# Optimization experiments

Measured on AMD Instinct MI355X. Metric: run time of the kernel, lower is better.

The kernel has to match this reference:

```python
import jax, jax.numpy as jnp
import numpy as np

D_MODEL = 1024
N_HEADS = 16
D_K = D_MODEL // N_HEADS
ROPE_THETA = 10000.0


def setup_inputs() -> dict:
    key = jax.random.key(0)
    ks = jax.random.split(key, 5)
    B, S = 2, 2048
    scale = 1.0 / np.sqrt(D_MODEL)
    return {
        "x": jax.random.normal(ks[0], (B, S, D_MODEL), dtype=jnp.float32),
        "token_positions": jnp.arange(S, dtype=jnp.int32),
        "Wq": jax.random.normal(ks[1], (D_MODEL, D_MODEL), dtype=jnp.float32) * scale,
        "Wk": jax.random.normal(ks[2], (D_MODEL, D_MODEL), dtype=jnp.float32) * scale,
        "Wv": jax.random.normal(ks[3], (D_MODEL, D_MODEL), dtype=jnp.float32) * scale,
        "Wo": jax.random.normal(ks[4], (D_MODEL, D_MODEL), dtype=jnp.float32) * scale,
    }


def apply_rope(x, positions):
    # x: [b, h, s, d_k]; interleaved-pair rotary embedding, theta=10000
    half = D_K // 2
    inv_freq = ROPE_THETA ** (-jnp.arange(0, half, dtype=x.dtype) * 2.0 / D_K)  # [half]
    angles = positions.astype(x.dtype)[:, None] * inv_freq[None, :]             # [s, half]
    cos, sin = jnp.cos(angles), jnp.sin(angles)                                 # [s, half]
    x1 = x[..., 0::2]
    x2 = x[..., 1::2]
    r1 = x1 * cos - x2 * sin
    r2 = x1 * sin + x2 * cos
    # re-interleave
    return jnp.stack([r1, r2], axis=-1).reshape(x.shape)


def reference(x, token_positions, Wq, Wk, Wv, Wo):
    B, S, _ = x.shape
    # Linear(d_model, d_model) with no bias: y = x @ W.T
    Q = jnp.einsum("bsd,ed->bse", x, Wq).reshape(B, S, N_HEADS, D_K).transpose(0, 2, 1, 3)
    K = jnp.einsum("bsd,ed->bse", x, Wk).reshape(B, S, N_HEADS, D_K).transpose(0, 2, 1, 3)
    V = jnp.einsum("bsd,ed->bse", x, Wv).reshape(B, S, N_HEADS, D_K).transpose(0, 2, 1, 3)
    Q = apply_rope(Q, token_positions)
    K = apply_rope(K, token_positions)
    scores = jnp.einsum("bhqd,bhkd->bhqk", Q, K) / jnp.sqrt(jnp.asarray(D_K, x.dtype))
    causal = jnp.tril(jnp.ones((S, S), dtype=bool))
    scores = jnp.where(causal[None, None, :, :], scores, jnp.asarray(-jnp.inf, x.dtype))
    attn = jax.nn.softmax(scores, axis=-1)
    out = jnp.einsum("bhqk,bhkd->bhqd", attn, V)            # [b, h, s, d_k]
    out = out.transpose(0, 2, 1, 3).reshape(B, S, D_MODEL)   # [b, s, d_model]
    return jnp.einsum("bsd,ed->bse", out, Wo)
```

## Files before the change

### kernel.cpp

```cpp
#include <hip/hip_runtime.h>
#include <hip/hip_bf16.h>
#include <math.h>

#define SEQ 2048
#define NH  16
#define DKH 64
#define DM  1024
#define MR  4096

using bf16x8 = __attribute__((ext_vector_type(8))) short;
using f32x4  = __attribute__((ext_vector_type(4))) float;

__device__ __forceinline__ ushort f2b(float f) {
  unsigned u = __float_as_uint(f);
  return (ushort)((u + 0x7fffu + ((u >> 16) & 1u)) >> 16);
}

__device__ __forceinline__ float exp2_fast(float x) {
  float r; asm("v_exp_f32 %0, %1" : "=v"(r) : "v"(x)); return r;
}

__device__ __forceinline__ unsigned cvt_pk(float lo, float hi) {
  __hip_bfloat162 h = __float22bfloat162_rn(float2{lo, hi});
  return *reinterpret_cast<unsigned*>(&h);
}

__device__ __forceinline__ void gll16(const void* g, void* l) {
  __builtin_amdgcn_global_load_lds(
      (const __attribute__((address_space(1))) void*)g,
      (__attribute__((address_space(3))) void*)l, 16, 0, 0);
}

__global__ __launch_bounds__(256) void cvt_all(
    const float* __restrict__ x,  const float* __restrict__ wq,
    const float* __restrict__ wk, const float* __restrict__ wv,
    const float* __restrict__ wo,
    ushort* __restrict__ xb,  ushort* __restrict__ wqb, ushort* __restrict__ wkb,
    ushort* __restrict__ wvb, ushort* __restrict__ wob)
{
  size_t e = ((size_t)blockIdx.x * 256 + threadIdx.x) * 4;
  const float* s; ushort* d; size_t off;
  if      (e < 4194304) { s = x;  d = xb;  off = e; }
  else if (e < 5242880) { s = wq; d = wqb; off = e - 4194304; }
  else if (e < 6291456) { s = wk; d = wkb; off = e - 5242880; }
  else if (e < 7340032) { s = wv; d = wvb; off = e - 6291456; }
  else                  { s = wo; d = wob; off = e - 7340032; }
  float4 f = *(const float4*)(s + off);
  ushort4 o4 = { f2b(f.x), f2b(f.y), f2b(f.z), f2b(f.w) };
  *(ushort4*)(d + off) = o4;
}

__global__ __launch_bounds__(512) void gemm_qkv(
    const ushort* __restrict__ X,
    const ushort* __restrict__ Wq, const ushort* __restrict__ Wk, const ushort* __restrict__ Wv,
    ushort* __restrict__ Q, ushort* __restrict__ K, ushort* __restrict__ Vt,
    const int* __restrict__ pos)
{
  __shared__ __align__(16) char As[2][16384];
  __shared__ __align__(16) char Bs[2][16384];

  const int id  = blockIdx.x;
  const int xcd = id & 7;
  const int i   = id >> 3;
  const int mt  = xcd * 4 + (i & 3);
  const int nt  = i >> 2;
  const int m0  = mt * 128;
  const int nG  = nt * 128;
  const int z   = nG >> 10;
  const int n0  = nG & 1023;
  const ushort* W = (z == 0) ? Wq : (z == 1) ? Wk : Wv;

  const int tid  = threadIdx.x;
  const int lane = tid & 63;
  const int w    = tid >> 6;
  const int wm   = (w >> 2) * 64;
  const int wn   = (w & 3) * 32;
  const int li   = lane & 15;
  const int g    = lane >> 4;

  f32x4 acc[4][2] = {};

  auto stage = [&](int t, int buf) {
    const int k0 = t * 64;
    #pragma unroll
    for (int it = 0; it < 2; ++it) {
      const int L  = w * 2048 + it * 1024 + lane * 16;
      const int r  = L >> 7;
      const int sc = ((L >> 4) & 7) ^ (r & 7);
      gll16(X + (size_t)(m0 + r) * DM + k0 + sc * 8, &As[buf][w * 2048 + it * 1024]);
      gll16(W + (size_t)(n0 + r) * DM + k0 + sc * 8, &Bs[buf][w * 2048 + it * 1024]);
    }
  };

  auto compute = [&](int buf) {
    #pragma unroll
    for (int ks = 0; ks < 2; ++ks) {
      bf16x8 af[4], bfr[2];
      #pragma unroll
      for (int mf = 0; mf < 4; ++mf) {
        const int row = wm + mf * 16 + li;
        af[mf] = *(const bf16x8*)(&As[buf][row * 128 + (((ks * 4 + g) ^ (row & 7)) << 4)]);
      }
      #pragma unroll
      for (int nf = 0; nf < 2; ++nf) {
        const int row = wn + nf * 16 + li;
        bfr[nf] = *(const bf16x8*)(&Bs[buf][row * 128 + (((ks * 4 + g) ^ (row & 7)) << 4)]);
      }
      #pragma unroll
      for (int mf = 0; mf < 4; ++mf)
        #pragma unroll
        for (int nf = 0; nf < 2; ++nf)
          acc[mf][nf] = __builtin_amdgcn_mfma_f32_16x16x32_bf16(af[mf], bfr[nf], acc[mf][nf], 0, 0, 0);
    }
  };

  stage(0, 0);
  for (int t = 0; t < 16; ++t) {
    if (t < 15) {
      stage(t + 1, (t + 1) & 1);
      __builtin_amdgcn_sched_barrier(0);
      asm volatile("s_waitcnt vmcnt(4)" ::: "memory");
    } else {
      asm volatile("s_waitcnt vmcnt(0)" ::: "memory");
    }
    __builtin_amdgcn_s_barrier();
    __builtin_amdgcn_sched_barrier(0);
    compute(t & 1);
    __builtin_amdgcn_sched_barrier(0);
    __builtin_amdgcn_s_barrier();
  }

  #pragma unroll
  for (int nf = 0; nf < 2; ++nf) {
    const int n = n0 + wn + nf * 16 + li;
    const int h = n >> 6;
    const int d = n & 63;
    if (z == 2) {
      #pragma unroll
      for (int mf = 0; mf < 4; ++mf) {
        const int m  = m0 + wm + mf * 16 + g * 4;
        const int b  = m >> 11;
        const int s2 = m & (SEQ - 1);
        ushort4 pk = { f2b(acc[mf][nf][0]), f2b(acc[mf][nf][1]),
                       f2b(acc[mf][nf][2]), f2b(acc[mf][nf][3]) };
        *(ushort4*)(Vt + (((size_t)b * NH + h) * DKH + d) * SEQ + s2) = pk;
      }
    } else {
      ushort* DST = (z == 0) ? Q : K;
      const float freq = __expf(-(float)(d >> 1) * 0.2878231366242557f);
      #pragma unroll
      for (int mf = 0; mf < 4; ++mf) {
        #pragma unroll
        for (int r = 0; r < 4; ++r) {
          const int m  = m0 + wm + mf * 16 + g * 4 + r;
          const int b  = m >> 11;
          const int s2 = m & (SEQ - 1);
          const float ang = (float)pos[s2] * freq;
          float sn, cs;
          __sincosf(ang, &sn, &cs);
          const float v1 = acc[mf][nf][r];
          const float v2 = __shfl_xor(v1, 1);
          float ov = (d & 1) ? (v2 * sn + v1 * cs)
                             : (v1 * cs - v2 * sn);
          if (z == 0) ov *= 0.1803368801111204f;
          DST[(((size_t)b * NH + h) * SEQ + s2) * DKH + d] = f2b(ov);
        }
      }
    }
  }
}

__global__ __launch_bounds__(512) void gemm_wo(
    const ushort* __restrict__ A, const ushort* __restrict__ W,
    float* __restrict__ out)
{
  __shared__ __align__(16) char As[2][16384];
  __shared__ __align__(16) char Bs[2][16384];

  const int id  = blockIdx.x;
  const int xcd = id & 7;
  const int i   = id >> 3;
  const int mt  = xcd * 4 + (i & 3);
  const int nt  = i >> 2;
  const int m0  = mt * 128;
  const int n0  = nt * 128;

  const int tid  = threadIdx.x;
  const int lane = tid & 63;
  const int w    = tid >> 6;
  const int wm   = (w >> 2) * 64;
  const int wn   = (w & 3) * 32;
  const int li   = lane & 15;
  const int g    = lane >> 4;

  f32x4 acc[4][2] = {};

  auto stage = [&](int t, int buf) {
    const int k0 = t * 64;
    #pragma unroll
    for (int it = 0; it < 2; ++it) {
      const int L  = w * 2048 + it * 1024 + lane * 16;
      const int r  = L >> 7;
      const int sc = ((L >> 4) & 7) ^ (r & 7);
      gll16(A + (size_t)(m0 + r) * DM + k0 + sc * 8, &As[buf][w * 2048 + it * 1024]);
      gll16(W + (size_t)(n0 + r) * DM + k0 + sc * 8, &Bs[buf][w * 2048 + it * 1024]);
    }
  };

  auto compute = [&](int buf) {
    #pragma unroll
    for (int ks = 0; ks < 2; ++ks) {
      bf16x8 af[4], bfr[2];
      #pragma unroll
      for (int mf = 0; mf < 4; ++mf) {
        const int row = wm + mf * 16 + li;
        af[mf] = *(const bf16x8*)(&As[buf][row * 128 + (((ks * 4 + g) ^ (row & 7)) << 4)]);
      }
      #pragma unroll
      for (int nf = 0; nf < 2; ++nf) {
        const int row = wn + nf * 16 + li;
        bfr[nf] = *(const bf16x8*)(&Bs[buf][row * 128 + (((ks * 4 + g) ^ (row & 7)) << 4)]);
      }
      #pragma unroll
      for (int mf = 0; mf < 4; ++mf)
        #pragma unroll
        for (int nf = 0; nf < 2; ++nf)
          acc[mf][nf] = __builtin_amdgcn_mfma_f32_16x16x32_bf16(af[mf], bfr[nf], acc[mf][nf], 0, 0, 0);
    }
  };

  stage(0, 0);
  for (int t = 0; t < 16; ++t) {
    if (t < 15) {
      stage(t + 1, (t + 1) & 1);
      __builtin_amdgcn_sched_barrier(0);
      asm volatile("s_waitcnt vmcnt(4)" ::: "memory");
    } else {
      asm volatile("s_waitcnt vmcnt(0)" ::: "memory");
    }
    __builtin_amdgcn_s_barrier();
    __builtin_amdgcn_sched_barrier(0);
    compute(t & 1);
    __builtin_amdgcn_sched_barrier(0);
    __builtin_amdgcn_s_barrier();
  }

  #pragma unroll
  for (int nf = 0; nf < 2; ++nf)
    #pragma unroll
    for (int mf = 0; mf < 4; ++mf)
      #pragma unroll
      for (int r = 0; r < 4; ++r)
        out[(size_t)(m0 + wm + mf * 16 + g * 4 + r) * DM + n0 + wn + nf * 16 + li] = acc[mf][nf][r];
}

__global__ __launch_bounds__(256) void attn(
    const ushort* __restrict__ Q, const ushort* __restrict__ K,
    const ushort* __restrict__ Vt, ushort* __restrict__ AO)
{
  __shared__ __align__(16) char Ks[8192];
  __shared__ __align__(16) char Vs[8192];
  __shared__ __align__(16) char Ps[8192];

  const int tid  = threadIdx.x;
  const int lane = tid & 63;
  const int w    = tid >> 6;
  const int li   = lane & 15;
  const int g    = lane >> 4;

  const int bx  = blockIdx.x;
  const int xcd = bx & 7;
  const int idx = bx >> 3;
  const int j   = idx >> 2;
  const int s   = idx & 3;
  const int qb  = (s & 1) ? (31 - j) : j;
  const int bh  = s * 8 + xcd;
  const int q0b = qb * 64;
  const int n   = qb + 1;
  const int q0w = q0b + w * 16;

  const ushort* Qb = Q  + (size_t)bh * SEQ * DKH;
  const ushort* Kb = K  + (size_t)bh * SEQ * DKH;
  const ushort* Vb = Vt + (size_t)bh * DKH * SEQ;
  char* Pw = Ps + w * 2048;

  const bf16x8 qf0 = *(const bf16x8*)(Qb + (size_t)(q0w + li) * DKH + g * 8);
  const bf16x8 qf1 = *(const bf16x8*)(Qb + (size_t)(q0w + li) * DKH + 32 + g * 8);

  f32x4 o[4] = {};
  float m_ = -INFINITY, l_ = 0.f;

  auto stage = [&](int kt) {
    const int k0 = kt * 64;
    #pragma unroll
    for (int it = 0; it < 2; ++it) {
      const int L  = w * 2048 + it * 1024 + lane * 16;
      const int r  = L >> 7;
      const int sc = ((L >> 4) & 7) ^ (r & 7);
      gll16(Kb + (size_t)(k0 + r) * DKH + sc * 8, Ks + w * 2048 + it * 1024);
      gll16(Vb + (size_t)r * SEQ + k0 + sc * 8,   Vs + w * 2048 + it * 1024);
    }
  };

  auto computeT = [&](int t, bool diag) {
    const int k0 = t * 64;

    f32x4 st[4] = {};
    __builtin_amdgcn_s_setprio(1);
    #pragma unroll
    for (int nf = 0; nf < 4; ++nf) {
      const int row = nf * 16 + li;
      bf16x8 kfa = *(const bf16x8*)(Ks + row * 128 + (((0 + g) ^ (row & 7)) << 4));
      bf16x8 kfb = *(const bf16x8*)(Ks + row * 128 + (((4 + g) ^ (row & 7)) << 4));
      st[nf] = __builtin_amdgcn_mfma_f32_16x16x32_bf16(kfa, qf0, st[nf], 0, 0, 0);
      st[nf] = __builtin_amdgcn_mfma_f32_16x16x32_bf16(kfb, qf1, st[nf], 0, 0, 0);
    }
    __builtin_amdgcn_s_setprio(0);

    if (diag) {
      #pragma unroll
      for (int nf = 0; nf < 4; ++nf)
        #pragma unroll
        for (int r = 0; r < 4; ++r)
          if (k0 + nf * 16 + g * 4 + r > q0w + li) st[nf][r] = -1e30f;
    }

    float mx = fmaxf(fmaxf(fmaxf(st[0][0], st[0][1]), fmaxf(st[0][2], st[0][3])),
                     fmaxf(fmaxf(st[1][0], st[1][1]), fmaxf(st[1][2], st[1][3])));
    mx = fmaxf(mx, fmaxf(fmaxf(fmaxf(st[2][0], st[2][1]), fmaxf(st[2][2], st[2][3])),
                         fmaxf(fmaxf(st[3][0], st[3][1]), fmaxf(st[3][2], st[3][3]))));
    mx = fmaxf(mx, __shfl_xor(mx, 16));
    mx = fmaxf(mx, __shfl_xor(mx, 32));

    const bool rescale = !__all(mx - m_ <= 8.0f);
    float al = 1.0f;
    if (rescale) {
      const float newm = fmaxf(m_, mx);
      al = exp2_fast(m_ - newm);
      m_ = newm;
    }

    float p[4][4];
    float rs = 0.f;
    #pragma unroll
    for (int nf = 0; nf < 4; ++nf)
      #pragma unroll
      for (int r = 0; r < 4; ++r) {
        p[nf][r] = exp2_fast(st[nf][r] - m_);
        rs += p[nf][r];
      }
    rs += __shfl_xor(rs, 16);
    rs += __shfl_xor(rs, 32);

    if (rescale) {
      l_ = l_ * al + rs;
      float alr[4];
      #pragma unroll
      for (int r = 0; r < 4; ++r) alr[r] = __shfl(al, g * 4 + r);
      #pragma unroll
      for (int nf = 0; nf < 4; ++nf)
        #pragma unroll
        for (int r = 0; r < 4; ++r) o[nf][r] *= alr[r];
    } else {
      l_ += rs;
    }

    #pragma unroll
    for (int nf = 0; nf < 4; ++nf) {
      uint2 pv = { cvt_pk(p[nf][0], p[nf][1]), cvt_pk(p[nf][2], p[nf][3]) };
      const int cw = nf * 2 + (g >> 1);
      *(uint2*)(Pw + li * 128 + ((cw ^ (li & 7)) << 4) + ((g & 1) << 3)) = pv;
    }
    bf16x8 pf0 = *(const bf16x8*)(Pw + li * 128 + (((0 + g) ^ (li & 7)) << 4));
    bf16x8 pf1 = *(const bf16x8*)(Pw + li * 128 + (((4 + g) ^ (li & 7)) << 4));

    __builtin_amdgcn_s_setprio(1);
    #pragma unroll
    for (int nf = 0; nf < 4; ++nf) {
      const int row = nf * 16 + li;
      bf16x8 vfa = *(const bf16x8*)(Vs + row * 128 + (((0 + g) ^ (row & 7)) << 4));
      bf16x8 vfb = *(const bf16x8*)(Vs + row * 128 + (((4 + g) ^ (row & 7)) << 4));
      o[nf] = __builtin_amdgcn_mfma_f32_16x16x32_bf16(pf0, vfa, o[nf], 0, 0, 0);
      o[nf] = __builtin_amdgcn_mfma_f32_16x16x32_bf16(pf1, vfb, o[nf], 0, 0, 0);
    }
    __builtin_amdgcn_s_setprio(0);
  };

  for (int t = 0; t < n; ++t) {
    stage(t);
    __syncthreads();
    computeT(t, t == n - 1);
    __syncthreads();
  }

  const float inv = 1.0f / l_;
  float ir[4];
  #pragma unroll
  for (int r = 0; r < 4; ++r) ir[r] = __shfl(inv, g * 4 + r);

  const int b = bh >> 4, h = bh & 15;
  #pragma unroll
  for (int nf = 0; nf < 4; ++nf)
    #pragma unroll
    for (int r = 0; r < 4; ++r) {
      const int q = q0w + g * 4 + r;
      AO[((size_t)b * SEQ + q) * DM + h * DKH + nf * 16 + li] = f2b(o[nf][r] * ir[r]);
    }
}

extern "C" void kernel_launch(void* const* d_in, const int* in_sizes, int n_in,
                              void* d_out, int out_size, void* d_ws, size_t ws_size,
                              hipStream_t stream)
{
  const float* x   = (const float*)d_in[0];
  const int*   pos = (const int*)  d_in[1];
  const float* Wq  = (const float*)d_in[2];
  const float* Wk  = (const float*)d_in[3];
  const float* Wv  = (const float*)d_in[4];
  const float* Wo  = (const float*)d_in[5];
  float* out = (float*)d_out;

  ushort* ws  = (ushort*)d_ws;
  ushort* xb  = ws;
  ushort* wqb = xb  + 4194304;
  ushort* wkb = wqb + 1048576;
  ushort* wvb = wkb + 1048576;
  ushort* wob = wvb + 1048576;
  ushort* Qb  = wob + 1048576;
  ushort* Kb  = Qb  + 4194304;
  ushort* Vtb = Kb  + 4194304;
  ushort* AOb = Vtb + 4194304;

  cvt_all<<<8192, 256, 0, stream>>>(x, Wq, Wk, Wv, Wo, xb, wqb, wkb, wvb, wob);
  gemm_qkv<<<768, 512, 0, stream>>>(xb, wqb, wkb, wvb, Qb, Kb, Vtb, pos);
  attn<<<1024, 256, 0, stream>>>(Qb, Kb, Vtb, AOb);
  gemm_wo<<<256, 512, 0, stream>>>(AOb, wob, out);
}
```

Baseline: 114.6 us.

## Split KV tiles across two wave groups per attention block and merge partial softmax

Doubles the attention block to 512 threads. The two 4-wave halves each process about half of the causal KV tiles for the same 64 query rows, using separate K/V LDS buffers. Afterwards the second half writes its partial O, max and sum to LDS, and the first half merges them with rescaled online-softmax weights before writing output. The aim is to shorten each block's serial KV loop and raise wave-level parallelism, at the cost of a larger LDS footprint (48KB per block), an extra merge step, and idle waves when the tile counts are odd.

```diff
diff --git a/kernel.cpp b/kernel.cpp
--- a/kernel.cpp
+++ b/kernel.cpp
@@ -254,17 +254,24 @@
         out[(size_t)(m0 + wm + mf * 16 + g * 4 + r) * DM + n0 + wn + nf * 16 + li] = acc[mf][nf][r];
 }
 
-__global__ __launch_bounds__(256) void attn(
+__global__ __launch_bounds__(512) void attn(
     const ushort* __restrict__ Q, const ushort* __restrict__ K,
     const ushort* __restrict__ Vt, ushort* __restrict__ AO)
 {
-  __shared__ __align__(16) char Ks[8192];
-  __shared__ __align__(16) char Vs[8192];
-  __shared__ __align__(16) char Ps[8192];
+  __shared__ __align__(16) char smem[49152];
+  char* KsA = smem;
+  char* VsA = smem + 8192;
+  char* KsH = smem + 16384;
+  char* VsH = smem + 24576;
+  char* Ps  = smem + 32768;
+  float* OmB = (float*)smem;
+  float* mlB = (float*)(smem + 16384);
 
   const int tid  = threadIdx.x;
   const int lane = tid & 63;
   const int w    = tid >> 6;
+  const int half = w >> 2;
+  const int wl   = w & 3;
   const int li   = lane & 15;
   const int g    = lane >> 4;
 
@@ -277,11 +284,17 @@
   const int bh  = s * 8 + xcd;
   const int q0b = qb * 64;
   const int n   = qb + 1;
-  const int q0w = q0b + w * 16;
+  const int nA  = (n + 1) >> 1;
+  const int nB  = n - nA;
+  const int myT0 = half ? nA : 0;
+  const int myN  = half ? nB : nA;
+  const int q0w = q0b + wl * 16;
 
   const ushort* Qb = Q  + (size_t)bh * SEQ * DKH;
   const ushort* Kb = K  + (size_t)bh * SEQ * DKH;
   const ushort* Vb = Vt + (size_t)bh * DKH * SEQ;
+  char* Kc = half ? KsH : KsA;
+  char* Vc = half ? VsH : VsA;
   char* Pw = Ps + w * 2048;
 
   const bf16x8 qf0 = *(const bf16x8*)(Qb + (size_t)(q0w + li) * DKH + g * 8);
@@ -294,11 +307,11 @@
     const int k0 = kt * 64;
     #pragma unroll
     for (int it = 0; it < 2; ++it) {
-      const int L  = w * 2048 + it * 1024 + lane * 16;
+      const int L  = wl * 2048 + it * 1024 + lane * 16;
       const int r  = L >> 7;
       const int sc = ((L >> 4) & 7) ^ (r & 7);
-      gll16(Kb + (size_t)(k0 + r) * DKH + sc * 8, Ks + w * 2048 + it * 1024);
-      gll16(Vb + (size_t)r * SEQ + k0 + sc * 8,   Vs + w * 2048 + it * 1024);
+      gll16(Kb + (size_t)(k0 + r) * DKH + sc * 8, Kc + wl * 2048 + it * 1024);
+      gll16(Vb + (size_t)r * SEQ + k0 + sc * 8,   Vc + wl * 2048 + it * 1024);
     }
   };
 
@@ -310,8 +323,8 @@
     #pragma unroll
     for (int nf = 0; nf < 4; ++nf) {
       const int row = nf * 16 + li;
-      bf16x8 kfa = *(const bf16x8*)(Ks + row * 128 + (((0 + g) ^ (row & 7)) << 4));
-      bf16x8 kfb = *(const bf16x8*)(Ks + row * 128 + (((4 + g) ^ (row & 7)) << 4));
+      bf16x8 kfa = *(const bf16x8*)(Kc + row * 128 + (((0 + g) ^ (row & 7)) << 4));
+      bf16x8 kfb = *(const bf16x8*)(Kc + row * 128 + (((4 + g) ^ (row & 7)) << 4));
       st[nf] = __builtin_amdgcn_mfma_f32_16x16x32_bf16(kfa, qf0, st[nf], 0, 0, 0);
       st[nf] = __builtin_amdgcn_mfma_f32_16x16x32_bf16(kfb, qf1, st[nf], 0, 0, 0);
     }
@@ -378,34 +391,58 @@
     #pragma unroll
     for (int nf = 0; nf < 4; ++nf) {
       const int row = nf * 16 + li;
-      bf16x8 vfa = *(const bf16x8*)(Vs + row * 128 + (((0 + g) ^ (row & 7)) << 4));
-      bf16x8 vfb = *(const bf16x8*)(Vs + row * 128 + (((4 + g) ^ (row & 7)) << 4));
+      bf16x8 vfa = *(const bf16x8*)(Vc + row * 128 + (((0 + g) ^ (row & 7)) << 4));
+      bf16x8 vfb = *(const bf16x8*)(Vc + row * 128 + (((4 + g) ^ (row & 7)) << 4));
       o[nf] = __builtin_amdgcn_mfma_f32_16x16x32_bf16(pf0, vfa, o[nf], 0, 0, 0);
       o[nf] = __builtin_amdgcn_mfma_f32_16x16x32_bf16(pf1, vfb, o[nf], 0, 0, 0);
     }
     __builtin_amdgcn_s_setprio(0);
   };
 
-  for (int t = 0; t < n; ++t) {
-    stage(t);
+  for (int t = 0; t < nA; ++t) {
+    if (t < myN) stage(myT0 + t);
     __syncthreads();
-    computeT(t, t == n - 1);
+    if (t < myN) computeT(myT0 + t, myT0 + t == n - 1);
     __syncthreads();
   }
 
-  const float inv = 1.0f / l_;
-  float ir[4];
-  #pragma unroll
-  for (int r = 0; r < 4; ++r) ir[r] = __shfl(inv, g * 4 + r);
-
-  const int b = bh >> 4, h = bh & 15;
-  #pragma unroll
-  for (int nf = 0; nf < 4; ++nf)
+  if (half) {
+    #pragma unroll
+    for (int nf = 0; nf < 4; ++nf)
+      *(f32x4*)&OmB[(wl * 64 + lane) * 16 + nf * 4] = o[nf];
+    mlB[(wl * 16 + li) * 2 + 0] = m_;
+    mlB[(wl * 16 + li) * 2 + 1] = l_;
+  }
+  __syncthreads();
+  if (!half) {
+    const float mB = mlB[(wl * 16 + li) * 2 + 0];
+    const float lB = mlB[(wl * 16 + li) * 2 + 1];
+    const float mN = fmaxf(m_, mB);
+    const float a  = exp2_fast(m_ - mN);
+    const float bs = exp2_fast(mB - mN);
+    const float lN = l_ * a + lB * bs;
+    const float inv = 1.0f / lN;
+
+    float ar[4], br[4], ir[4];
     #pragma unroll
     for (int r = 0; r < 4; ++r) {
-      const int q = q0w + g * 4 + r;
-      AO[((size_t)b * SEQ + q) * DM + h * DKH + nf * 16 + li] = f2b(o[nf][r] * ir[r]);
-    }
+      ar[r] = __shfl(a,   g * 4 + r);
+      br[r] = __shfl(bs,  g * 4 + r);
+      ir[r] = __shfl(inv, g * 4 + r);
+    }
+
+    const int b = bh >> 4, h = bh & 15;
+    #pragma unroll
+    for (int nf = 0; nf < 4; ++nf) {
+      const f32x4 ob = *(const f32x4*)&OmB[(wl * 64 + lane) * 16 + nf * 4];
+      #pragma unroll
+      for (int r = 0; r < 4; ++r) {
+        const int q = q0w + g * 4 + r;
+        const float v = (o[nf][r] * ar[r] + ob[r] * br[r]) * ir[r];
+        AO[((size_t)b * SEQ + q) * DM + h * DKH + nf * 16 + li] = f2b(v);
+      }
+    }
+  }
 }
 
 extern "C" void kernel_launch(void* const* d_in, const int* in_sizes, int n_in,
@@ -433,6 +470,6 @@
 
   cvt_all<<<8192, 256, 0, stream>>>(x, Wq, Wk, Wv, Wo, xb, wqb, wkb, wvb, wob);
   gemm_qkv<<<768, 512, 0, stream>>>(xb, wqb, wkb, wvb, Qb, Kb, Vtb, pos);
-  attn<<<1024, 256, 0, stream>>>(Qb, Kb, Vtb, AOb);
+  attn<<<1024, 512, 0, stream>>>(Qb, Kb, Vtb, AOb);
   gemm_wo<<<256, 512, 0, stream>>>(AOb, wob, out);
 }
```

New measurement: 125.4 us. 9.4% more time.

## Give each attention wave two 16-row query fragments with 128-thread blocks

Applied to the files above, without the earlier changes.

The attention kernel now runs 2 waves per block instead of 4, and each wave handles 32 query rows as two 16-row fragments. Each K/V fragment read from LDS then feeds two MFMAs, which halves LDS read traffic per unit of compute and doubles the staging work each wave does. In exchange, register pressure rises (two accumulators and two score sets per wave) and each block has fewer waves to hide latency behind the per-tile barriers.

```diff
diff --git a/kernel.cpp b/kernel.cpp
--- a/kernel.cpp
+++ b/kernel.cpp
@@ -254,7 +254,7 @@
         out[(size_t)(m0 + wm + mf * 16 + g * 4 + r) * DM + n0 + wn + nf * 16 + li] = acc[mf][nf][r];
 }
 
-__global__ __launch_bounds__(256) void attn(
+__global__ __launch_bounds__(128) void attn(
     const ushort* __restrict__ Q, const ushort* __restrict__ K,
     const ushort* __restrict__ Vt, ushort* __restrict__ AO)
 {
@@ -277,102 +277,116 @@
   const int bh  = s * 8 + xcd;
   const int q0b = qb * 64;
   const int n   = qb + 1;
-  const int q0w = q0b + w * 16;
+  const int q0w = q0b + w * 32;
 
   const ushort* Qb = Q  + (size_t)bh * SEQ * DKH;
   const ushort* Kb = K  + (size_t)bh * SEQ * DKH;
   const ushort* Vb = Vt + (size_t)bh * DKH * SEQ;
-  char* Pw = Ps + w * 2048;
-
-  const bf16x8 qf0 = *(const bf16x8*)(Qb + (size_t)(q0w + li) * DKH + g * 8);
-  const bf16x8 qf1 = *(const bf16x8*)(Qb + (size_t)(q0w + li) * DKH + 32 + g * 8);
-
-  f32x4 o[4] = {};
-  float m_ = -INFINITY, l_ = 0.f;
+
+  bf16x8 qfA[2], qfB[2];
+  #pragma unroll
+  for (int f = 0; f < 2; ++f) {
+    const ushort* qr = Qb + (size_t)(q0w + f * 16 + li) * DKH;
+    qfA[f] = *(const bf16x8*)(qr + g * 8);
+    qfB[f] = *(const bf16x8*)(qr + 32 + g * 8);
+  }
+
+  f32x4 o[2][4] = {};
+  float m_[2] = { -INFINITY, -INFINITY };
+  float l_[2] = { 0.f, 0.f };
 
   auto stage = [&](int kt) {
     const int k0 = kt * 64;
     #pragma unroll
-    for (int it = 0; it < 2; ++it) {
-      const int L  = w * 2048 + it * 1024 + lane * 16;
+    for (int it = 0; it < 4; ++it) {
+      const int L  = w * 4096 + it * 1024 + lane * 16;
       const int r  = L >> 7;
       const int sc = ((L >> 4) & 7) ^ (r & 7);
-      gll16(Kb + (size_t)(k0 + r) * DKH + sc * 8, Ks + w * 2048 + it * 1024);
-      gll16(Vb + (size_t)r * SEQ + k0 + sc * 8,   Vs + w * 2048 + it * 1024);
+      gll16(Kb + (size_t)(k0 + r) * DKH + sc * 8, Ks + w * 4096 + it * 1024);
+      gll16(Vb + (size_t)r * SEQ + k0 + sc * 8,   Vs + w * 4096 + it * 1024);
     }
   };
 
   auto computeT = [&](int t, bool diag) {
     const int k0 = t * 64;
 
-    f32x4 st[4] = {};
+    f32x4 st[2][4] = {};
     __builtin_amdgcn_s_setprio(1);
     #pragma unroll
     for (int nf = 0; nf < 4; ++nf) {
       const int row = nf * 16 + li;
       bf16x8 kfa = *(const bf16x8*)(Ks + row * 128 + (((0 + g) ^ (row & 7)) << 4));
       bf16x8 kfb = *(const bf16x8*)(Ks + row * 128 + (((4 + g) ^ (row & 7)) << 4));
-      st[nf] = __builtin_amdgcn_mfma_f32_16x16x32_bf16(kfa, qf0, st[nf], 0, 0, 0);
-      st[nf] = __builtin_amdgcn_mfma_f32_16x16x32_bf16(kfb, qf1, st[nf], 0, 0, 0);
+      st[0][nf] = __builtin_amdgcn_mfma_f32_16x16x32_bf16(kfa, qfA[0], st[0][nf], 0, 0, 0);
+      st[0][nf] = __builtin_amdgcn_mfma_f32_16x16x32_bf16(kfb, qfB[0], st[0][nf], 0, 0, 0);
+      st[1][nf] = __builtin_amdgcn_mfma_f32_16x16x32_bf16(kfa, qfA[1], st[1][nf], 0, 0, 0);
+      st[1][nf] = __builtin_amdgcn_mfma_f32_16x16x32_bf16(kfb, qfB[1], st[1][nf], 0, 0, 0);
     }
     __builtin_amdgcn_s_setprio(0);
 
-    if (diag) {
+    bf16x8 pf0[2], pf1[2];
+    #pragma unroll
+    for (int f = 0; f < 2; ++f) {
+      const int q0f = q0w + f * 16;
+
+      if (diag) {
+        #pragma unroll
+        for (int nf = 0; nf < 4; ++nf)
+          #pragma unroll
+          for (int r = 0; r < 4; ++r)
+            if (k0 + nf * 16 + g * 4 + r > q0f + li) st[f][nf][r] = -1e30f;
+      }
+
+      float mx = fmaxf(fmaxf(fmaxf(st[f][0][0], st[f][0][1]), fmaxf(st[f][0][2], st[f][0][3])),
+                       fmaxf(fmaxf(st[f][1][0], st[f][1][1]), fmaxf(st[f][1][2], st[f][1][3])));
+      mx = fmaxf(mx, fmaxf(fmaxf(fmaxf(st[f][2][0], st[f][2][1]), fmaxf(st[f][2][2], st[f][2][3])),
+                           fmaxf(fmaxf(st[f][3][0], st[f][3][1]), fmaxf(st[f][3][2], st[f][3][3]))));
+      mx = fmaxf(mx, __shfl_xor(mx, 16));
+      mx = fmaxf(mx, __shfl_xor(mx, 32));
+
+      const bool rescale = !__all(mx - m_[f] <= 8.0f);
+      float al = 1.0f;
+      if (rescale) {
+        const float newm = fmaxf(m_[f], mx);
+        al = exp2_fast(m_[f] - newm);
+        m_[f] = newm;
+      }
+
+      float p[4][4];
+      float rs = 0.f;
       #pragma unroll
       for (int nf = 0; nf < 4; ++nf)
         #pragma unroll
-        for (int r = 0; r < 4; ++r)
-          if (k0 + nf * 16 + g * 4 + r > q0w + li) st[nf][r] = -1e30f;
-    }
-
-    float mx = fmaxf(fmaxf(fmaxf(st[0][0], st[0][1]), fmaxf(st[0][2], st[0][3])),
-                     fmaxf(fmaxf(st[1][0], st[1][1]), fmaxf(st[1][2], st[1][3])));
-    mx = fmaxf(mx, fmaxf(fmaxf(fmaxf(st[2][0], st[2][1]), fmaxf(st[2][2], st[2][3])),
-                         fmaxf(fmaxf(st[3][0], st[3][1]), fmaxf(st[3][2], st[3][3]))));
-    mx = fmaxf(mx, __shfl_xor(mx, 16));
-    mx = fmaxf(mx, __shfl_xor(mx, 32));
-
-    const bool rescale = !__all(mx - m_ <= 8.0f);
-    float al = 1.0f;
-    if (rescale) {
-      const float newm = fmaxf(m_, mx);
-      al = exp2_fast(m_ - newm);
-      m_ = newm;
-    }
-
-    float p[4][4];
-    float rs = 0.f;
-    #pragma unroll
-    for (int nf = 0; nf < 4; ++nf)
-      #pragma unroll
-      for (int r = 0; r < 4; ++r) {
-        p[nf][r] = exp2_fast(st[nf][r] - m_);
-        rs += p[nf][r];
-      }
-    rs += __shfl_xor(rs, 16);
-    rs += __shfl_xor(rs, 32);
-
-    if (rescale) {
-      l_ = l_ * al + rs;
-      float alr[4];
-      #pragma unroll
-      for (int r = 0; r < 4; ++r) alr[r] = __shfl(al, g * 4 + r);
-      #pragma unroll
-      for (int nf = 0; nf < 4; ++nf)
-        #pragma unroll
-        for (int r = 0; r < 4; ++r) o[nf][r] *= alr[r];
-    } else {
-      l_ += rs;
-    }
-
-    #pragma unroll
-    for (int nf = 0; nf < 4; ++nf) {
-      uint2 pv = { cvt_pk(p[nf][0], p[nf][1]), cvt_pk(p[nf][2], p[nf][3]) };
-      const int cw = nf * 2 + (g >> 1);
-      *(uint2*)(Pw + li * 128 + ((cw ^ (li & 7)) << 4) + ((g & 1) << 3)) = pv;
-    }
-    bf16x8 pf0 = *(const bf16x8*)(Pw + li * 128 + (((0 + g) ^ (li & 7)) << 4));
-    bf16x8 pf1 = *(const bf16x8*)(Pw + li * 128 + (((4 + g) ^ (li & 7)) << 4));
+        for (int r = 0; r < 4; ++r) {
+          p[nf][r] = exp2_fast(st[f][nf][r] - m_[f]);
+          rs += p[nf][r];
+        }
+      rs += __shfl_xor(rs, 16);
+      rs += __shfl_xor(rs, 32);
+
+      if (rescale) {
+        l_[f] = l_[f] * al + rs;
+        float alr[4];
+        #pragma unroll
+        for (int r = 0; r < 4; ++r) alr[r] = __shfl(al, g * 4 + r);
+        #pragma unroll
+        for (int nf = 0; nf < 4; ++nf)
+          #pragma unroll
+          for (int r = 0; r < 4; ++r) o[f][nf][r] *= alr[r];
+      } else {
+        l_[f] += rs;
+      }
+
+      char* Pw = Ps + w * 4096 + f * 2048;
+      #pragma unroll
+      for (int nf = 0; nf < 4; ++nf) {
+        uint2 pv = { cvt_pk(p[nf][0], p[nf][1]), cvt_pk(p[nf][2], p[nf][3]) };
+        const int cw = nf * 2 + (g >> 1);
+        *(uint2*)(Pw + li * 128 + ((cw ^ (li & 7)) << 4) + ((g & 1) << 3)) = pv;
+      }
+      pf0[f] = *(const bf16x8*)(Pw + li * 128 + (((0 + g) ^ (li & 7)) << 4));
+      pf1[f] = *(const bf16x8*)(Pw + li * 128 + (((4 + g) ^ (li & 7)) << 4));
+    }
 
     __builtin_amdgcn_s_setprio(1);
     #pragma unroll
@@ -380,8 +394,10 @@
       const int row = nf * 16 + li;
       bf16x8 vfa = *(const bf16x8*)(Vs + row * 128 + (((0 + g) ^ (row & 7)) << 4));
       bf16x8 vfb = *(const bf16x8*)(Vs + row * 128 + (((4 + g) ^ (row & 7)) << 4));
-      o[nf] = __builtin_amdgcn_mfma_f32_16x16x32_bf16(pf0, vfa, o[nf], 0, 0, 0);
-      o[nf] = __builtin_amdgcn_mfma_f32_16x16x32_bf16(pf1, vfb, o[nf], 0, 0, 0);
+      o[0][nf] = __builtin_amdgcn_mfma_f32_16x16x32_bf16(pf0[0], vfa, o[0][nf], 0, 0, 0);
+      o[0][nf] = __builtin_amdgcn_mfma_f32_16x16x32_bf16(pf1[0], vfb, o[0][nf], 0, 0, 0);
+      o[1][nf] = __builtin_amdgcn_mfma_f32_16x16x32_bf16(pf0[1], vfa, o[1][nf], 0, 0, 0);
+      o[1][nf] = __builtin_amdgcn_mfma_f32_16x16x32_bf16(pf1[1], vfb, o[1][nf], 0, 0, 0);
     }
     __builtin_amdgcn_s_setprio(0);
   };
@@ -393,19 +409,21 @@
     __syncthreads();
   }
 
-  const float inv = 1.0f / l_;
-  float ir[4];
+  const int b = bh >> 4, hh = bh & 15;
   #pragma unroll
-  for (int r = 0; r < 4; ++r) ir[r] = __shfl(inv, g * 4 + r);
-
-  const int b = bh >> 4, h = bh & 15;
-  #pragma unroll
-  for (int nf = 0; nf < 4; ++nf)
-    #pragma unroll
-    for (int r = 0; r < 4; ++r) {
-      const int q = q0w + g * 4 + r;
-      AO[((size_t)b * SEQ + q) * DM + h * DKH + nf * 16 + li] = f2b(o[nf][r] * ir[r]);
-    }
+  for (int f = 0; f < 2; ++f) {
+    const float inv = 1.0f / l_[f];
+    float ir[4];
+    #pragma unroll
+    for (int r = 0; r < 4; ++r) ir[r] = __shfl(inv, g * 4 + r);
+    #pragma unroll
+    for (int nf = 0; nf < 4; ++nf)
+      #pragma unroll
+      for (int r = 0; r < 4; ++r) {
+        const int q = q0w + f * 16 + g * 4 + r;
+        AO[((size_t)b * SEQ + q) * DM + hh * DKH + nf * 16 + li] = f2b(o[f][nf][r] * ir[r]);
+      }
+  }
 }
 
 extern "C" void kernel_launch(void* const* d_in, const int* in_sizes, int n_in,
@@ -433,6 +451,6 @@
 
   cvt_all<<<8192, 256, 0, stream>>>(x, Wq, Wk, Wv, Wo, xb, wqb, wkb, wvb, wob);
   gemm_qkv<<<768, 512, 0, stream>>>(xb, wqb, wkb, wvb, Qb, Kb, Vtb, pos);
-  attn<<<1024, 256, 0, stream>>>(Qb, Kb, Vtb, AOb);
+  attn<<<1024, 128, 0, stream>>>(Qb, Kb, Vtb, AOb);
   gemm_wo<<<256, 512, 0, stream>>>(AOb, wob, out);
 }
```

Measured after the change: 131.5 us. 14.8% more time.
